# Kernel tuning notes

Hardware: AMD Instinct MI355X
Metric: run time of the kernel (lower is better)

Reference implementation:

```python
import jax, jax.numpy as jnp
import numpy as np

K_SIZE = 3
STRIDE = 1
DIL = 1
PAD = (K_SIZE - 1) // 2 * DIL          # padding of the deformable conv
OFF_PAD = (K_SIZE - 1) // 2            # padding of the offset conv
KK = K_SIZE * K_SIZE


def setup_inputs() -> dict:
    key = jax.random.key(0)
    k1, k2, k3, k4 = jax.random.split(key, 4)
    B, C, H, W = 4, 256, 64, 64
    O = 256
    x = jax.random.normal(k1, (B, C, H, W), jnp.float32)
    # offset/mask conv params (small so sampled offsets stay in a realistic range)
    w_off = jax.random.normal(k2, (3 * KK, C, K_SIZE, K_SIZE), jnp.float32) * 0.01
    b_off = jax.random.normal(k3, (3 * KK,), jnp.float32) * 0.01
    # deformable conv weight (conv_dcn has bias=False in the source)
    w_dcn = jax.random.normal(k4, (O, C, K_SIZE, K_SIZE), jnp.float32) * (1.0 / np.sqrt(C * KK))
    return {"x": x, "w_off": w_off, "b_off": b_off, "w_dcn": w_dcn}


def _bilinear_sample(x, ys, xs):
    """x: [B,C,H,W]; ys, xs: [B,KK,Ho,Wo] fractional coords. Zero outside bounds.
    Returns [B,C,KK,Ho,Wo]."""
    B, C, H, W = x.shape
    _, K, Ho, Wo = ys.shape
    y0 = jnp.floor(ys)
    x0 = jnp.floor(xs)
    y1, x1 = y0 + 1.0, x0 + 1.0
    wy1 = ys - y0
    wy0 = 1.0 - wy1
    wx1 = xs - x0
    wx0 = 1.0 - wx1
    x_flat = x.reshape(B, C, H * W)

    def gather_term(yi, xi, wt):
        valid = (yi >= 0) & (yi < H) & (xi >= 0) & (xi < W)
        yc = jnp.clip(yi, 0, H - 1).astype(jnp.int32)
        xc = jnp.clip(xi, 0, W - 1).astype(jnp.int32)
        idx = (yc * W + xc).reshape(B, -1)                      # [B, K*Ho*Wo]
        g = jax.vmap(lambda xf, i: xf[:, i])(x_flat, idx)       # [B, C, K*Ho*Wo]
        w = (wt * valid.astype(wt.dtype)).reshape(B, 1, -1)
        return g * w

    out = (gather_term(y0, x0, wy0 * wx0)
           + gather_term(y0, x1, wy0 * wx1)
           + gather_term(y1, x0, wy1 * wx0)
           + gather_term(y1, x1, wy1 * wx1))
    return out.reshape(B, C, K, Ho, Wo)


def _dcn_v2(x, w_off, b_off, w_dcn):
    B, C, H, W = x.shape
    # offset/mask conv (standard conv, padding (k-1)//2)
    om = jax.lax.conv_general_dilated(
        x, w_off, (STRIDE, STRIDE), [(OFF_PAD, OFF_PAD)] * 2,
        dimension_numbers=("NCHW", "OIHW", "NCHW")) + b_off[None, :, None, None]
    offset = om[:, :2 * KK]                 # [B, 2*KK, Ho, Wo] as (dy0,dx0,dy1,dx1,...)
    mask = jax.nn.sigmoid(om[:, 2 * KK:])   # [B, KK, Ho, Wo]
    Ho, Wo = offset.shape[2], offset.shape[3]

    off = offset.reshape(B, KK, 2, Ho, Wo)
    off_y, off_x = off[:, :, 0], off[:, :, 1]

    kh = (jnp.arange(KK) // K_SIZE).astype(jnp.float32)
    kw = (jnp.arange(KK) % K_SIZE).astype(jnp.float32)
    py = (jnp.arange(Ho) * STRIDE - PAD).astype(jnp.float32)
    px = (jnp.arange(Wo) * STRIDE - PAD).astype(jnp.float32)

    ys = py[None, None, :, None] + (kh * DIL)[None, :, None, None] + off_y
    xs = px[None, None, None, :] + (kw * DIL)[None, :, None, None] + off_x

    sampled = _bilinear_sample(x, ys, xs)           # [B,C,KK,Ho,Wo]
    sampled = sampled * mask[:, None]               # modulated (DCNv2)
    w = w_dcn.reshape(w_dcn.shape[0], C, KK)
    return jnp.einsum("bckhw,ock->bohw", sampled, w)


def reference(x, w_off, b_off, w_dcn):
    return _dcn_v2(x, w_off, b_off, w_dcn)
```

## Files before the change

kernel.cpp:

```cpp
#include <hip/hip_runtime.h>

typedef __attribute__((ext_vector_type(8))) short short8;
typedef __attribute__((ext_vector_type(4))) float f32x4;

#define CIN 256
#define OUTC 256
#define HWW 4096
#define IMG_H 64
#define IMG_W 64
#define SROW 264

__device__ __forceinline__ short f2bf(float f) {
    unsigned u = __float_as_uint(f);
    u += 0x7fffu + ((u >> 16) & 1u);
    return (short)(u >> 16);
}
__device__ __forceinline__ float bf2f(short s) {
    return __uint_as_float(((unsigned)(unsigned short)s) << 16);
}

__global__ __launch_bounds__(256) void prep(const float* __restrict__ x,
                                            const float* __restrict__ w_dcn,
                                            const float* __restrict__ w_off,
                                            short* __restrict__ xT,
                                            short* __restrict__ wF,
                                            short* __restrict__ wFo) {
    int bid = blockIdx.x;
    if (bid < 1024) {
        __shared__ float T[64][65];
        int p0 = (bid & 63) * 64;
        int c0 = ((bid >> 6) & 3) * 64;
        int b  = bid >> 8;
        int j = threadIdx.x & 63, i = threadIdx.x >> 6;
        const float* xb = x + ((size_t)b * CIN + c0) * HWW + p0;
#pragma unroll
        for (int k = 0; k < 16; ++k) {
            int row = i * 16 + k;
            T[row][j] = xb[(size_t)row * HWW + j];
        }
        __syncthreads();
        short* xTb = xT + ((size_t)b * HWW + p0) * CIN + c0;
#pragma unroll
        for (int k = 0; k < 16; ++k) {
            int prow = i * 16 + k;
            xTb[(size_t)prow * CIN + j] = f2bf(T[j][prow]);
        }
    } else if (bid < 1312) {
        int g = (bid - 1024) * 256 + threadIdx.x;
        int lane = g & 63;
        int rest = g >> 6;
        int octile = rest & 15;
        int step = rest >> 4;
        int kp = step >> 3, chv = step & 7;
        int oc = octile * 16 + (lane & 15);
        int cbase = chv * 32 + (lane >> 4) * 8;
        short8 v;
#pragma unroll
        for (int j = 0; j < 8; ++j)
            v[j] = f2bf(w_dcn[oc * 2304 + (cbase + j) * 9 + kp]);
        *(short8*)(wF + (size_t)g * 8) = v;
    } else {
        int g = (bid - 1312) * 256 + threadIdx.x;
        int lane = g & 63;
        int rest = g >> 6;
        int octile = rest & 1;
        int step = rest >> 1;
        int kp = step >> 3, chv = step & 7;
        int oc = octile * 16 + (lane & 15);
        int cbase = chv * 32 + (lane >> 4) * 8;
        short8 v;
#pragma unroll
        for (int j = 0; j < 8; ++j)
            v[j] = (oc < 27) ? f2bf(w_off[(oc * 256 + cbase + j) * 9 + kp]) : (short)0;
        *(short8*)(wFo + (size_t)g * 8) = v;
    }
}

__global__ __launch_bounds__(256) void offs_mfma(
        const short* __restrict__ xT, const short* __restrict__ wFo,
        float* __restrict__ P) {
    __shared__ short Sm[2][32 * SROW];

    int tid = threadIdx.x;
    int d = blockIdx.x;
    int L = (d & 7) * 64 + (d >> 3);
    int b = L >> 7;
    int ph = L & 127;
    int pbase = ph * 32;
    int prow = ph >> 1;
    int pc0 = (ph & 1) * 32;
    const short* xTb = xT + (size_t)b * HWW * CIN;

    int lane = tid & 63, wave = tid >> 6;
    int fr = lane & 15, fq = lane >> 4;
    int octile = wave & 1, pxt = wave >> 1;

    short8 st[4];

    auto loads = [&](int kp) {
        int yy = prow - 1 + kp / 3;
        int dx = kp % 3 - 1;
#pragma unroll
        for (int it = 0; it < 4; ++it) {
            int item = tid + it * 256;
            int cg8 = item & 31, px = item >> 5;
            int xx = pc0 + px + dx;
            bool ok = (yy >= 0 && yy < IMG_H && xx >= 0 && xx < IMG_W);
            int idx = ok ? ((yy * IMG_W + xx) * CIN + cg8 * 8) : 0;
            short8 v = *(const short8*)&xTb[idx];
            if (!ok) v = (short8){0,0,0,0,0,0,0,0};
            st[it] = v;
        }
    };
    auto writes = [&](int bufi) {
#pragma unroll
        for (int it = 0; it < 4; ++it) {
            int item = tid + it * 256;
            int cg8 = item & 31, px = item >> 5;
            *(short8*)&Sm[bufi][px * SROW + cg8 * 8] = st[it];
        }
    };

    f32x4 acc = (f32x4){0.f, 0.f, 0.f, 0.f};

    loads(0); writes(0);
    __syncthreads();
    for (int kp = 0; kp < 9; ++kp) {
        short8 aF[8];
#pragma unroll
        for (int chv = 0; chv < 8; ++chv)
            aF[chv] = *(const short8*)(wFo +
                    (((size_t)((kp * 8 + chv) * 2 + octile)) * 64 + lane) * 8);
        if (kp < 8) loads(kp + 1);
        const short* SmB = Sm[kp & 1];
#pragma unroll
        for (int chv = 0; chv < 8; ++chv) {
            short8 bF = *(const short8*)&SmB[(pxt * 16 + fr) * SROW + chv * 32 + fq * 8];
            acc = __builtin_amdgcn_mfma_f32_16x16x32_bf16(aF[chv], bF, acc, 0, 0, 0);
        }
        if (kp < 8) writes((kp + 1) & 1);
        __syncthreads();
    }

#pragma unroll
    for (int r = 0; r < 4; ++r) {
        int oc = octile * 16 + fq * 4 + r;
        if (oc < 27)
            P[((size_t)b * 32 + oc) * HWW + pbase + pxt * 16 + fr] = acc[r];
    }
}

__global__ __launch_bounds__(512, 2) void dcn_main(
        const short* __restrict__ xT, const float* __restrict__ b_off,
        const float* __restrict__ P, const short* __restrict__ wF,
        float* __restrict__ out) {
    __shared__ short Sm[2][64 * SROW];
    __shared__ float4 preW[576];
    __shared__ int4  preI[576];

    int tid = threadIdx.x;
    int d = blockIdx.x;
    int L = (d & 7) * 32 + (d >> 3);
    int b = L >> 6;
    int row = L & 63;
    int pbase = row * 64;
    const short* xTb = xT + (size_t)b * HWW * CIN;

    for (int e = tid; e < 576; e += 512) {
        int px = e & 63, kp = e >> 6;
        int p = pbase + px;
        float oy = P[((size_t)b * 32 + 2 * kp) * HWW + p] + b_off[2 * kp];
        float ox = P[((size_t)b * 32 + 2 * kp + 1) * HWW + p] + b_off[2 * kp + 1];
        float ml = P[((size_t)b * 32 + 18 + kp) * HWW + p] + b_off[18 + kp];
        float m = 1.0f / (1.0f + expf(-ml));
        float ys = (float)(row - 1 + kp / 3) + oy;
        float xs = (float)(px - 1 + kp % 3) + ox;
        float y0f = floorf(ys), x0f = floorf(xs);
        float fy = ys - y0f, fx = xs - x0f;
        int iy0 = (int)y0f, ix0 = (int)x0f;
        int iy1 = iy0 + 1, ix1 = ix0 + 1;
        float vy0 = (iy0 >= 0 && iy0 < IMG_H) ? 1.f : 0.f;
        float vy1 = (iy1 >= 0 && iy1 < IMG_H) ? 1.f : 0.f;
        float vx0 = (ix0 >= 0 && ix0 < IMG_W) ? 1.f : 0.f;
        float vx1 = (ix1 >= 0 && ix1 < IMG_W) ? 1.f : 0.f;
        int ry0 = min(max(iy0, 0), IMG_H - 1) * IMG_W;
        int ry1 = min(max(iy1, 0), IMG_H - 1) * IMG_W;
        int cx0 = min(max(ix0, 0), IMG_W - 1);
        int cx1 = min(max(ix1, 0), IMG_W - 1);
        float wy0 = 1.f - fy, wy1 = fy, wx0 = 1.f - fx, wx1 = fx;
        preW[e] = make_float4(wy0 * wx0 * vy0 * vx0 * m, wy0 * wx1 * vy0 * vx1 * m,
                              wy1 * wx0 * vy1 * vx0 * m, wy1 * wx1 * vy1 * vx1 * m);
        preI[e] = make_int4((ry0 + cx0) * CIN, (ry0 + cx1) * CIN,
                            (ry1 + cx0) * CIN, (ry1 + cx1) * CIN);
    }
    __syncthreads();

    int lane = tid & 63, wave = tid >> 6;
    int fr = lane & 15, fq = lane >> 4;

    short8 st[4][4];

    auto loads = [&](int kp) {
#pragma unroll
        for (int it = 0; it < 4; ++it) {
            int item = tid + it * 512;
            int cg8 = item & 31, px = item >> 5;
            int4 iv = preI[kp * 64 + px];
            int co = cg8 * 8;
            st[it][0] = *(const short8*)&xTb[iv.x + co];
            st[it][1] = *(const short8*)&xTb[iv.y + co];
            st[it][2] = *(const short8*)&xTb[iv.z + co];
            st[it][3] = *(const short8*)&xTb[iv.w + co];
        }
    };
    auto writes = [&](int kp, int bufi) {
#pragma unroll
        for (int it = 0; it < 4; ++it) {
            int item = tid + it * 512;
            int cg8 = item & 31, px = item >> 5;
            float4 wv = preW[kp * 64 + px];
            short8 o;
#pragma unroll
            for (int j = 0; j < 8; ++j) {
                float v = wv.x * bf2f(st[it][0][j]) + wv.y * bf2f(st[it][1][j]) +
                          wv.z * bf2f(st[it][2][j]) + wv.w * bf2f(st[it][3][j]);
                o[j] = f2bf(v);
            }
            *(short8*)&Sm[bufi][px * SROW + cg8 * 8] = o;
        }
    };

    f32x4 acc[2][4];
#pragma unroll
    for (int m = 0; m < 2; ++m)
#pragma unroll
        for (int n = 0; n < 4; ++n)
            acc[m][n] = (f32x4){0.f, 0.f, 0.f, 0.f};

    loads(0); writes(0, 0);
    __syncthreads();
    for (int kp = 0; kp < 9; ++kp) {
        short8 aF[16];
#pragma unroll
        for (int chv = 0; chv < 8; ++chv)
#pragma unroll
            for (int m = 0; m < 2; ++m)
                aF[chv * 2 + m] = *(const short8*)(wF +
                        (((size_t)((kp * 8 + chv) * 16 + wave * 2 + m)) * 64 + lane) * 8);
        if (kp < 8) loads(kp + 1);
        const short* SmB = Sm[kp & 1];
#pragma unroll
        for (int chv = 0; chv < 8; ++chv)
#pragma unroll
            for (int n = 0; n < 4; ++n) {
                short8 bF = *(const short8*)&SmB[(n * 16 + fr) * SROW + chv * 32 + fq * 8];
#pragma unroll
                for (int m = 0; m < 2; ++m)
                    acc[m][n] = __builtin_amdgcn_mfma_f32_16x16x32_bf16(
                            aF[chv * 2 + m], bF, acc[m][n], 0, 0, 0);
            }
        if (kp < 8) writes(kp + 1, (kp + 1) & 1);
        __syncthreads();
    }

    float* outb = out + (size_t)b * (OUTC * HWW) + pbase;
#pragma unroll
    for (int m = 0; m < 2; ++m)
#pragma unroll
        for (int n = 0; n < 4; ++n)
#pragma unroll
            for (int r = 0; r < 4; ++r)
                outb[(size_t)(wave * 32 + m * 16 + fq * 4 + r) * HWW + n * 16 + fr] =
                        acc[m][n][r];
}

extern "C" void kernel_launch(void* const* d_in, const int* in_sizes, int n_in,
                              void* d_out, int out_size, void* d_ws, size_t ws_size,
                              hipStream_t stream) {
    const float* x     = (const float*)d_in[0];
    const float* w_off = (const float*)d_in[1];
    const float* b_off = (const float*)d_in[2];
    const float* w_dcn = (const float*)d_in[3];
    float* out = (float*)d_out;

    short* xT  = (short*)d_ws;
    float* P   = (float*)(xT + (size_t)4 * HWW * CIN);
    short* wF  = (short*)(P + (size_t)4 * 32 * HWW);
    short* wFo = wF + (size_t)73728 * 8;

    prep<<<1348, 256, 0, stream>>>(x, w_dcn, w_off, xT, wF, wFo);
    offs_mfma<<<512, 256, 0, stream>>>(xT, wFo, P);
    dcn_main<<<256, 512, 0, stream>>>(xT, b_off, P, wF, out);
}
```

Measured before the change: 63.29 us.

## Restructure DCN main GEMM to 32x32 MFMA with split-K waves and swizzled LDS

Reworks dcn_main to run 1024 threads per block, with 16 waves split into 8 output-channel groups and 2 K-halves. Each wave uses 32x32x16 bf16 MFMAs, and the two K-halves are reduced through LDS before the store. The LDS tile drops its padding in favour of an XOR swizzle to avoid bank conflicts, and gather indices are stored as ushort4 to save LDS. The weight prepacking is reordered to match the new fragment layout. The intent is more MFMA work per fragment load and more latency hiding; the cost is an extra LDS reduction pass, one block per CU, and higher register pressure under the 1024-thread bound.

```diff
diff --git a/kernel.cpp b/kernel.cpp
--- a/kernel.cpp
+++ b/kernel.cpp
@@ -2,6 +2,7 @@
 
 typedef __attribute__((ext_vector_type(8))) short short8;
 typedef __attribute__((ext_vector_type(4))) float f32x4;
+typedef __attribute__((ext_vector_type(16))) float f32x16;
 
 #define CIN 256
 #define OUTC 256
@@ -49,11 +50,11 @@
         int g = (bid - 1024) * 256 + threadIdx.x;
         int lane = g & 63;
         int rest = g >> 6;
-        int octile = rest & 15;
-        int step = rest >> 4;
-        int kp = step >> 3, chv = step & 7;
-        int oc = octile * 16 + (lane & 15);
-        int cbase = chv * 32 + (lane >> 4) * 8;
+        int og = rest & 7;
+        int kidx = rest >> 3;
+        int kp = kidx >> 4, kc = kidx & 15;
+        int oc = og * 32 + (lane & 31);
+        int cbase = kc * 16 + (lane >> 5) * 8;
         short8 v;
 #pragma unroll
         for (int j = 0; j < 8; ++j)
@@ -150,13 +151,13 @@
     }
 }
 
-__global__ __launch_bounds__(512, 2) void dcn_main(
+__global__ __launch_bounds__(1024) void dcn_main(
         const short* __restrict__ xT, const float* __restrict__ b_off,
         const float* __restrict__ P, const short* __restrict__ wF,
         float* __restrict__ out) {
-    __shared__ short Sm[2][64 * SROW];
-    __shared__ float4 preW[576];
-    __shared__ int4  preI[576];
+    __shared__ short Sm[2][64 * 256];
+    __shared__ float4  preW[576];
+    __shared__ ushort4 preI[576];
 
     int tid = threadIdx.x;
     int d = blockIdx.x;
@@ -166,7 +167,8 @@
     int pbase = row * 64;
     const short* xTb = xT + (size_t)b * HWW * CIN;
 
-    for (int e = tid; e < 576; e += 512) {
+    if (tid < 576) {
+        int e = tid;
         int px = e & 63, kp = e >> 6;
         int p = pbase + px;
         float oy = P[((size_t)b * 32 + 2 * kp) * HWW + p] + b_off[2 * kp];
@@ -190,34 +192,35 @@
         float wy0 = 1.f - fy, wy1 = fy, wx0 = 1.f - fx, wx1 = fx;
         preW[e] = make_float4(wy0 * wx0 * vy0 * vx0 * m, wy0 * wx1 * vy0 * vx1 * m,
                               wy1 * wx0 * vy1 * vx0 * m, wy1 * wx1 * vy1 * vx1 * m);
-        preI[e] = make_int4((ry0 + cx0) * CIN, (ry0 + cx1) * CIN,
-                            (ry1 + cx0) * CIN, (ry1 + cx1) * CIN);
+        preI[e] = make_ushort4((unsigned short)(ry0 + cx0), (unsigned short)(ry0 + cx1),
+                               (unsigned short)(ry1 + cx0), (unsigned short)(ry1 + cx1));
     }
     __syncthreads();
 
     int lane = tid & 63, wave = tid >> 6;
-    int fr = lane & 15, fq = lane >> 4;
-
-    short8 st[4][4];
+    int og = wave & 7, kh = wave >> 3;
+    int pxl = lane & 31, hl = lane >> 5, sw = lane & 15;
+
+    int i_cg8 = tid & 31, i_px = tid >> 5;
+
+    short8 st[2][4];
 
     auto loads = [&](int kp) {
 #pragma unroll
-        for (int it = 0; it < 4; ++it) {
-            int item = tid + it * 512;
-            int cg8 = item & 31, px = item >> 5;
-            int4 iv = preI[kp * 64 + px];
-            int co = cg8 * 8;
-            st[it][0] = *(const short8*)&xTb[iv.x + co];
-            st[it][1] = *(const short8*)&xTb[iv.y + co];
-            st[it][2] = *(const short8*)&xTb[iv.z + co];
-            st[it][3] = *(const short8*)&xTb[iv.w + co];
+        for (int it = 0; it < 2; ++it) {
+            int px = i_px + it * 32;
+            ushort4 iv = preI[kp * 64 + px];
+            int co = i_cg8 * 8;
+            st[it][0] = *(const short8*)&xTb[(int)iv.x * CIN + co];
+            st[it][1] = *(const short8*)&xTb[(int)iv.y * CIN + co];
+            st[it][2] = *(const short8*)&xTb[(int)iv.z * CIN + co];
+            st[it][3] = *(const short8*)&xTb[(int)iv.w * CIN + co];
         }
     };
     auto writes = [&](int kp, int bufi) {
 #pragma unroll
-        for (int it = 0; it < 4; ++it) {
-            int item = tid + it * 512;
-            int cg8 = item & 31, px = item >> 5;
+        for (int it = 0; it < 2; ++it) {
+            int px = i_px + it * 32;
             float4 wv = preW[kp * 64 + px];
             short8 o;
 #pragma unroll
@@ -226,52 +229,63 @@
                           wv.z * bf2f(st[it][2][j]) + wv.w * bf2f(st[it][3][j]);
                 o[j] = f2bf(v);
             }
-            *(short8*)&Sm[bufi][px * SROW + cg8 * 8] = o;
+            *(short8*)&Sm[bufi][px * 256 + ((i_cg8 ^ (px & 15)) * 8)] = o;
         }
     };
 
-    f32x4 acc[2][4];
-#pragma unroll
-    for (int m = 0; m < 2; ++m)
-#pragma unroll
-        for (int n = 0; n < 4; ++n)
-            acc[m][n] = (f32x4){0.f, 0.f, 0.f, 0.f};
+    f32x16 acc[2];
+#pragma unroll
+    for (int n = 0; n < 2; ++n)
+#pragma unroll
+        for (int r = 0; r < 16; ++r)
+            acc[n][r] = 0.f;
 
     loads(0); writes(0, 0);
     __syncthreads();
     for (int kp = 0; kp < 9; ++kp) {
-        short8 aF[16];
-#pragma unroll
-        for (int chv = 0; chv < 8; ++chv)
-#pragma unroll
-            for (int m = 0; m < 2; ++m)
-                aF[chv * 2 + m] = *(const short8*)(wF +
-                        (((size_t)((kp * 8 + chv) * 16 + wave * 2 + m)) * 64 + lane) * 8);
+        short8 aF[8];
+#pragma unroll
+        for (int kc = 0; kc < 8; ++kc)
+            aF[kc] = *(const short8*)(wF +
+                    (((size_t)((kp * 16 + kh * 8 + kc) * 8 + og)) * 64 + lane) * 8);
         if (kp < 8) loads(kp + 1);
         const short* SmB = Sm[kp & 1];
 #pragma unroll
-        for (int chv = 0; chv < 8; ++chv)
-#pragma unroll
-            for (int n = 0; n < 4; ++n) {
-                short8 bF = *(const short8*)&SmB[(n * 16 + fr) * SROW + chv * 32 + fq * 8];
-#pragma unroll
-                for (int m = 0; m < 2; ++m)
-                    acc[m][n] = __builtin_amdgcn_mfma_f32_16x16x32_bf16(
-                            aF[chv * 2 + m], bF, acc[m][n], 0, 0, 0);
+        for (int kc = 0; kc < 8; ++kc) {
+            int chunkb = (kh * 8 + kc) * 2 + hl;
+#pragma unroll
+            for (int n = 0; n < 2; ++n) {
+                int px = n * 32 + pxl;
+                short8 bF = *(const short8*)&SmB[px * 256 + ((chunkb ^ sw) * 8)];
+                acc[n] = __builtin_amdgcn_mfma_f32_32x32x16_bf16(aF[kc], bF, acc[n], 0, 0, 0);
             }
+        }
         if (kp < 8) writes(kp + 1, (kp + 1) & 1);
         __syncthreads();
     }
 
-    float* outb = out + (size_t)b * (OUTC * HWW) + pbase;
-#pragma unroll
-    for (int m = 0; m < 2; ++m)
-#pragma unroll
-        for (int n = 0; n < 4; ++n)
-#pragma unroll
-            for (int r = 0; r < 4; ++r)
-                outb[(size_t)(wave * 32 + m * 16 + fq * 4 + r) * HWW + n * 16 + fr] =
-                        acc[m][n][r];
+    float* SmF = (float*)Sm;
+    if (kh == 1) {
+#pragma unroll
+        for (int n = 0; n < 2; ++n)
+#pragma unroll
+            for (int r = 0; r < 16; ++r) {
+                int ocr = (r & 3) + 8 * (r >> 2) + 4 * hl;
+                SmF[og * 2048 + ocr * 64 + n * 32 + pxl] = acc[n][r];
+            }
+    }
+    __syncthreads();
+    if (kh == 0) {
+        float* outb = out + (size_t)b * (OUTC * HWW) + (size_t)og * 32 * HWW + pbase;
+#pragma unroll
+        for (int n = 0; n < 2; ++n)
+#pragma unroll
+            for (int r = 0; r < 16; ++r) {
+                int ocr = (r & 3) + 8 * (r >> 2) + 4 * hl;
+                float v = acc[n][r] + SmF[og * 2048 + ocr * 64 + n * 32 + pxl];
+                outb[(size_t)ocr * HWW + n * 32 + pxl] = v;
+            }
+    }
 }
 
 extern "C" void kernel_launch(void* const* d_in, const int* in_sizes, int n_in,
@@ -290,5 +304,5 @@
 
     prep<<<1348, 256, 0, stream>>>(x, w_dcn, w_off, xT, wF, wFo);
     offs_mfma<<<512, 256, 0, stream>>>(xT, wFo, P);
-    dcn_main<<<256, 512, 0, stream>>>(xT, b_off, P, wF, out);
-}
+    dcn_main<<<256, 1024, 0, stream>>>(xT, b_off, P, wF, out);
+}
```

Measured after the change: 62.26 us. No clear change (-1.6%).

## Swizzle LDS staging layout, add sched barriers, fully unroll tap loop

Applied to the files above, without the earlier changes.

Changes the shared-memory staging tile from a padded row layout to a chunk-major layout with an XOR swizzle on pixel index, so both the combine writes and the MFMA B-fragment reads avoid bank conflicts without padding. It inserts scheduling barriers to keep global gathers, MFMAs and combine/writes in separate phases and fully unrolls the 9-tap loop. It also drops the min-2-blocks launch bound, which may let register usage grow at the cost of occupancy.

```diff
diff --git a/kernel.cpp b/kernel.cpp
--- a/kernel.cpp
+++ b/kernel.cpp
@@ -9,6 +9,7 @@
 #define IMG_H 64
 #define IMG_W 64
 #define SROW 264
+#define SB __builtin_amdgcn_sched_barrier(0)
 
 __device__ __forceinline__ short f2bf(float f) {
     unsigned u = __float_as_uint(f);
@@ -150,11 +151,11 @@
     }
 }
 
-__global__ __launch_bounds__(512, 2) void dcn_main(
+__global__ __launch_bounds__(512) void dcn_main(
         const short* __restrict__ xT, const float* __restrict__ b_off,
         const float* __restrict__ P, const short* __restrict__ wF,
         float* __restrict__ out) {
-    __shared__ short Sm[2][64 * SROW];
+    __shared__ short Sm[2][32 * 64 * 8];
     __shared__ float4 preW[576];
     __shared__ int4  preI[576];
 
@@ -197,36 +198,37 @@
 
     int lane = tid & 63, wave = tid >> 6;
     int fr = lane & 15, fq = lane >> 4;
-
-    short8 st[4][4];
-
-    auto loads = [&](int kp) {
+    int chunk = tid & 31, p0 = tid >> 5;
+    int co = chunk * 8;
+
+    auto soff = [](int s, int px) { return (s * 64 + (px & 32) + ((px & 31) ^ s)) * 8; };
+
+    short8 stO[4][4];
+
+    auto stage_loads = [&](int kq) {
 #pragma unroll
         for (int it = 0; it < 4; ++it) {
-            int item = tid + it * 512;
-            int cg8 = item & 31, px = item >> 5;
-            int4 iv = preI[kp * 64 + px];
-            int co = cg8 * 8;
-            st[it][0] = *(const short8*)&xTb[iv.x + co];
-            st[it][1] = *(const short8*)&xTb[iv.y + co];
-            st[it][2] = *(const short8*)&xTb[iv.z + co];
-            st[it][3] = *(const short8*)&xTb[iv.w + co];
+            int px = p0 + it * 16;
+            int4 iv = preI[kq * 64 + px];
+            stO[it][0] = *(const short8*)&xTb[iv.x + co];
+            stO[it][1] = *(const short8*)&xTb[iv.y + co];
+            stO[it][2] = *(const short8*)&xTb[iv.z + co];
+            stO[it][3] = *(const short8*)&xTb[iv.w + co];
         }
     };
-    auto writes = [&](int kp, int bufi) {
+    auto combine_writes = [&](int kq, int bufi) {
 #pragma unroll
         for (int it = 0; it < 4; ++it) {
-            int item = tid + it * 512;
-            int cg8 = item & 31, px = item >> 5;
-            float4 wv = preW[kp * 64 + px];
+            int px = p0 + it * 16;
+            float4 wv = preW[kq * 64 + px];
             short8 o;
 #pragma unroll
             for (int j = 0; j < 8; ++j) {
-                float v = wv.x * bf2f(st[it][0][j]) + wv.y * bf2f(st[it][1][j]) +
-                          wv.z * bf2f(st[it][2][j]) + wv.w * bf2f(st[it][3][j]);
+                float v = wv.x * bf2f(stO[it][0][j]) + wv.y * bf2f(stO[it][1][j]) +
+                          wv.z * bf2f(stO[it][2][j]) + wv.w * bf2f(stO[it][3][j]);
                 o[j] = f2bf(v);
             }
-            *(short8*)&Sm[bufi][px * SROW + cg8 * 8] = o;
+            *(short8*)&Sm[bufi][soff(chunk, px)] = o;
         }
     };
 
@@ -237,29 +239,38 @@
         for (int n = 0; n < 4; ++n)
             acc[m][n] = (f32x4){0.f, 0.f, 0.f, 0.f};
 
-    loads(0); writes(0, 0);
+    stage_loads(0);
+    SB;
+    combine_writes(0, 0);
     __syncthreads();
+
+#pragma unroll
     for (int kp = 0; kp < 9; ++kp) {
-        short8 aF[16];
+        short8 aFc[16];
 #pragma unroll
         for (int chv = 0; chv < 8; ++chv)
 #pragma unroll
             for (int m = 0; m < 2; ++m)
-                aF[chv * 2 + m] = *(const short8*)(wF +
+                aFc[chv * 2 + m] = *(const short8*)(wF +
                         (((size_t)((kp * 8 + chv) * 16 + wave * 2 + m)) * 64 + lane) * 8);
-        if (kp < 8) loads(kp + 1);
-        const short* SmB = Sm[kp & 1];
-#pragma unroll
-        for (int chv = 0; chv < 8; ++chv)
-#pragma unroll
-            for (int n = 0; n < 4; ++n) {
-                short8 bF = *(const short8*)&SmB[(n * 16 + fr) * SROW + chv * 32 + fq * 8];
-#pragma unroll
-                for (int m = 0; m < 2; ++m)
-                    acc[m][n] = __builtin_amdgcn_mfma_f32_16x16x32_bf16(
-                            aF[chv * 2 + m], bF, acc[m][n], 0, 0, 0);
-            }
-        if (kp < 8) writes(kp + 1, (kp + 1) & 1);
+        SB;
+        if (kp < 8) stage_loads(kp + 1);
+        SB;
+        {
+            const short* SmB = Sm[kp & 1];
+#pragma unroll
+            for (int chv = 0; chv < 8; ++chv)
+#pragma unroll
+                for (int n = 0; n < 4; ++n) {
+                    short8 bF = *(const short8*)&SmB[soff(chv * 4 + fq, n * 16 + fr)];
+#pragma unroll
+                    for (int m = 0; m < 2; ++m)
+                        acc[m][n] = __builtin_amdgcn_mfma_f32_16x16x32_bf16(
+                                aFc[chv * 2 + m], bF, acc[m][n], 0, 0, 0);
+                }
+        }
+        SB;
+        if (kp < 8) combine_writes(kp + 1, (kp + 1) & 1);
         __syncthreads();
     }
 
```

Result: no change. 62.21 us (-1.7%).
